# Kernel tuning notes

Measured on AMD Instinct MI355X. Metric: run time of the kernel, lower is better.

## Reference

```python
import jax, jax.numpy as jnp
import numpy as np

N_POINTS = 4096
N_PROJS = 2000


def setup_inputs() -> dict:
    key = jax.random.key(0)
    k1, k2, k3 = jax.random.split(key, 3)
    Xs = jax.random.normal(k1, (N_POINTS, 3), dtype=jnp.float32)
    Xt = jax.random.normal(k2, (N_POINTS, 3), dtype=jnp.float32)
    Us = jax.random.normal(k3, (N_PROJS, 3, 2), dtype=jnp.float32)
    return {"Xs": Xs, "Xt": Xt, "Us": Us}


def _project_to_circle(X, Us):
    # X: [n, d], Us: [P, d, 2] -> angles in [0, 1): [P, n]
    Xp = jnp.einsum('pdk,nd->pnk', Us, X)  # [P, n, 2]
    nrm = jnp.sqrt(jnp.sum(Xp * Xp, axis=-1, keepdims=True))
    Xp = Xp / jnp.maximum(nrm, 1e-12)  # F.normalize
    return (jnp.arctan2(-Xp[..., 1], -Xp[..., 0]) + np.pi) / (2 * np.pi)


def _emd1d_circle_p1(u_values, v_values):
    # Circular W1 via level-median (Delon et al.). u,v: [P, n], [P, m]
    P, n = u_values.shape
    m = v_values.shape[-1]
    dt = u_values.dtype
    u_w = jnp.full((P, n), 1.0 / n, dtype=dt)
    v_w = jnp.full((P, m), 1.0 / m, dtype=dt)
    us = jnp.sort(u_values, axis=-1)
    vs = jnp.sort(v_values, axis=-1)
    vals = jnp.concatenate([us, vs], axis=-1)            # [P, n+m]
    sorter = jnp.argsort(vals, axis=-1)
    vals_sorted = jnp.take_along_axis(vals, sorter, axis=-1)
    w_cat = jnp.concatenate([u_w, -v_w], axis=-1)
    cdf_diff = jnp.cumsum(jnp.take_along_axis(w_cat, sorter, axis=-1), axis=-1)
    cdf_sorter = jnp.argsort(cdf_diff, axis=-1)
    cdf_diff_sorted = jnp.take_along_axis(cdf_diff, cdf_sorter, axis=-1)
    vals_pad = jnp.concatenate([vals_sorted, jnp.ones((P, 1), dtype=dt)], axis=-1)
    delta = vals_pad[..., 1:] - vals_pad[..., :-1]
    weight_sorted = jnp.take_along_axis(delta, cdf_sorter, axis=-1)
    sum_weights = jnp.cumsum(weight_sorted, axis=-1) - 0.5
    sum_weights = jnp.where(sum_weights < 0, jnp.inf, sum_weights)
    inds = jnp.argmin(sum_weights, axis=-1)
    levMed = jnp.take_along_axis(cdf_diff_sorted, inds[:, None], axis=-1)  # [P, 1]
    return jnp.sum(delta * jnp.abs(cdf_diff - levMed), axis=-1)  # [P]


def reference(Xs, Xt, Us):
    Xps = _project_to_circle(Xs, Us)  # [P, n]
    Xpt = _project_to_circle(Xt, Us)  # [P, m]
    w1 = _emd1d_circle_p1(Xps, Xpt)
    return jnp.mean(w1)
```

## Files before the change

kernel.cpp:

```cpp
#include <hip/hip_runtime.h>
#include <math.h>

#define NPTS   4096
#define NPROJ  2000
#define NB     1024
#define NMERGE 8192
#define VPT    8

__device__ __forceinline__ int sw(int i) {
    return i ^ ((i >> 5) & 31);
}

__device__ __forceinline__ void local_merge(float v[VPT], bool asc) {
    #pragma unroll
    for (int j = 4; j >= 1; j >>= 1) {
        #pragma unroll
        for (int e = 0; e < VPT; ++e) {
            if ((e & j) == 0) {
                float a = v[e], b = v[e | j];
                float mn = fminf(a, b), mx = fmaxf(a, b);
                v[e]     = asc ? mn : mx;
                v[e | j] = asc ? mx : mn;
            }
        }
    }
}

__global__ __launch_bounds__(NB) void swd_kernel(
    const float* __restrict__ Xs, const float* __restrict__ Xt,
    const float* __restrict__ Us, float* __restrict__ out)
{
    __shared__ float keys[NMERGE];

    const int tid  = threadIdx.x;
    const int arr  = tid >> 9;
    const int c    = tid & 511;
    const int lane = tid & 63;
    const int wid  = tid >> 6;
    const int p    = blockIdx.x;

    const float u00 = Us[p*6+0], u01 = Us[p*6+1];
    const float u10 = Us[p*6+2], u11 = Us[p*6+3];
    const float u20 = Us[p*6+4], u21 = Us[p*6+5];

    const float pi_f   = 3.14159265358979323846f;
    const float inv2pi = 0.15915494309189535f;

    const float* __restrict__ X = arr ? Xt : Xs;

    float v[VPT];
    {
        const float4* X4 = (const float4*)(X + c * (VPT * 3));
        #pragma unroll
        for (int t = 0; t < 2; ++t) {
            float4 q0 = X4[t*3+0], q1 = X4[t*3+1], q2 = X4[t*3+2];
            #define ANG(x,y,z) ((atan2f(-((x)*u01+(y)*u11+(z)*u21), \
                                        -((x)*u00+(y)*u10+(z)*u20)) + pi_f) * inv2pi)
            v[t*4+0] = ANG(q0.x, q0.y, q0.z);
            v[t*4+1] = ANG(q0.w, q1.x, q1.y);
            v[t*4+2] = ANG(q1.z, q1.w, q2.x);
            v[t*4+3] = ANG(q2.y, q2.z, q2.w);
            #undef ANG
        }
    }

    #pragma unroll
    for (int k = 2; k <= 4; k <<= 1) {
        #pragma unroll
        for (int j = k >> 1; j >= 1; j >>= 1) {
            #pragma unroll
            for (int e = 0; e < VPT; ++e) {
                if ((e & j) == 0) {
                    bool asc = ((e & k) == 0);
                    float a = v[e], b = v[e | j];
                    float mn = fminf(a, b), mx = fmaxf(a, b);
                    v[e]     = asc ? mn : mx;
                    v[e | j] = asc ? mx : mn;
                }
            }
        }
    }

    local_merge(v, (c & 1) == 0);

    #pragma unroll
    for (int k = 16; k <= 512; k <<= 1) {
        bool asc = (k == 512) || ((c & (k >> 3)) == 0);
        #pragma unroll
        for (int d = k >> 4; d >= 1; d >>= 1) {
            bool keepmin = (((c & d) == 0) == asc);
            #pragma unroll
            for (int e = 0; e < VPT; ++e) {
                float o = __shfl_xor(v[e], d, 64);
                v[e] = keepmin ? fminf(v[e], o) : fmaxf(v[e], o);
            }
        }
        local_merge(v, asc);
    }

    #pragma unroll
    for (int e = 0; e < VPT; ++e) keys[sw(tid * VPT + e)] = v[e];
    __syncthreads();

    #define MERGE_ROUND(L, AB, DD)                                          \
    {                                                                       \
        const int Ab = (AB);                                                \
        const int Bb = Ab + (L);                                            \
        const int dd = (DD);                                                \
        int lo = dd > (L) ? dd - (L) : 0;                                   \
        int hi = dd < (L) ? dd : (L);                                       \
        while (lo < hi) {                                                   \
            int mid = (lo + hi) >> 1;                                       \
            if (keys[sw(Ab + mid)] <= keys[sw(Bb + (dd - 1 - mid))])        \
                lo = mid + 1; else hi = mid;                                \
        }                                                                   \
        int i = lo, j = dd - lo;                                            \
        const float INFV = __builtin_inff();                                \
        float cu = (i < (L)) ? keys[sw(Ab + i)] : INFV;                     \
        float cv = (j < (L)) ? keys[sw(Bb + j)] : INFV;                     \
        _Pragma("unroll")                                                   \
        for (int s = 0; s < VPT; ++s) {                                     \
            bool take = (cu <= cv);                                         \
            v[s] = fminf(cu, cv);                                           \
            if (take) { ++i; cu = (i < (L)) ? keys[sw(Ab + i)] : INFV; }    \
            else      { ++j; cv = (j < (L)) ? keys[sw(Bb + j)] : INFV; }    \
        }                                                                   \
        __syncthreads();                                                    \
        _Pragma("unroll")                                                   \
        for (int e = 0; e < VPT; ++e) keys[sw(tid * VPT + e)] = v[e];       \
        __syncthreads();                                                    \
    }

    MERGE_ROUND(512,  arr * 4096 + (c >> 7) * 1024, (c & 127) * VPT)
    MERGE_ROUND(1024, arr * 4096 + (c >> 8) * 2048, (c & 255) * VPT)
    MERGE_ROUND(2048, arr * 4096,                   c * VPT)
    #undef MERGE_ROUND

    int c_init;
    int offmin = 16, offmax = -16;
    float offf[VPT];
    {
        const int d0 = tid * VPT;
        int lo = d0 > NPTS ? d0 - NPTS : 0;
        int hi = d0 < NPTS ? d0 : NPTS;
        while (lo < hi) {
            int mid = (lo + hi) >> 1;
            if (keys[sw(mid)] <= keys[sw(NPTS + (d0 - 1 - mid))]) lo = mid + 1; else hi = mid;
        }
        int i = lo, j = d0 - lo;
        c_init = i - j;
        const float FMAXV = 3.402823466e+38f;
        float cu = (i < NPTS) ? keys[sw(i)] : FMAXV;
        float cv = (j < NPTS) ? keys[sw(NPTS + j)] : FMAXV;
        #pragma unroll
        for (int s = 0; s < VPT; ++s) {
            float cur;
            if (cu <= cv) { cur = cu; ++i; cu = (i < NPTS) ? keys[sw(i)] : FMAXV; }
            else          { cur = cv; ++j; cv = (j < NPTS) ? keys[sw(NPTS + j)] : FMAXV; }
            float nxt = fminf(cu, cv);
            if (nxt == FMAXV) nxt = 1.0f;
            v[s] = nxt - cur;
            int off = (i - j) - c_init;
            offmin = min(offmin, off);
            offmax = max(offmax, off);
            offf[s] = (float)off;
        }
    }

    __syncthreads();
    int*   ired = (int*)keys;
    float* red  = keys + 32;
    float* wred = keys + 48;

    int cmn = c_init + offmin, cmx = c_init + offmax;
    #pragma unroll
    for (int o = 32; o >= 1; o >>= 1) {
        cmn = min(cmn, __shfl_xor(cmn, o, 64));
        cmx = max(cmx, __shfl_xor(cmx, o, 64));
    }
    if (lane == 0) { ired[wid] = cmn; ired[16 + wid] = cmx; }
    if (tid < 16) red[tid] = 0.0f;
    __syncthreads();
    cmn = ired[0]; cmx = ired[16];
    #pragma unroll
    for (int w = 1; w < 16; ++w) {
        cmn = min(cmn, ired[w]);
        cmx = max(cmx, ired[16 + w]);
    }

    int lo_c = cmn - 1, hi_c = cmx;
    int it = 0;
    #pragma unroll 1
    while (hi_c - lo_c > 1) {
        const int mid = (lo_c + hi_c) >> 1;
        const float thrf = (float)(mid - c_init);
        float s_loc = 0.0f;
        #pragma unroll
        for (int s = 0; s < VPT; ++s)
            s_loc += (offf[s] <= thrf) ? v[s] : 0.0f;
        #pragma unroll
        for (int o = 32; o >= 1; o >>= 1) s_loc += __shfl_down(s_loc, o, 64);
        if (lane == 0) atomicAdd(&red[it], s_loc);
        __syncthreads();
        float S = red[it];
        if (S >= 0.5f) hi_c = mid; else lo_c = mid;
        ++it;
    }
    const int cstar = hi_c;

    float part = 0.0f;
    {
        const float thrf = (float)(cstar - c_init);
        #pragma unroll
        for (int s = 0; s < VPT; ++s)
            part += v[s] * fabsf(offf[s] - thrf);
    }
    #pragma unroll
    for (int o = 32; o >= 1; o >>= 1) part += __shfl_down(part, o, 64);
    if (lane == 0) wred[wid] = part;
    __syncthreads();
    if (tid == 0) {
        float w1 = 0.0f;
        #pragma unroll
        for (int w = 0; w < 16; ++w) w1 += wred[w];
        w1 *= (1.0f / 4096.0f);
        atomicAdd(out, w1 * (1.0f / (float)NPROJ));
    }
}

extern "C" void kernel_launch(void* const* d_in, const int* in_sizes, int n_in,
                              void* d_out, int out_size, void* d_ws, size_t ws_size,
                              hipStream_t stream) {
    const float* Xs = (const float*)d_in[0];
    const float* Xt = (const float*)d_in[1];
    const float* Us = (const float*)d_in[2];
    float* out = (float*)d_out;

    hipMemsetAsync(out, 0, sizeof(float), stream);
    swd_kernel<<<NPROJ, NB, 0, stream>>>(Xs, Xt, Us, out);
}
```

Before: 222.2 us.

## Double-buffer shared merge arrays and make merge-path loads branchless

Replaces the single shared key buffer with two ping-pong buffers, so each merge round reads from one and writes to the other. This removes one barrier per round and the barrier before the reduction scratch reuse. The merge-path step loops now do a single unconditional masked LDS load with selects instead of divergent branches with two load sites. The cost is doubling LDS to 64KB per block, which may limit residency on the CU.

Measured after the change: 217.8 us. 2.0% less time.

```diff
diff --git a/kernel.cpp b/kernel.cpp
--- a/kernel.cpp
+++ b/kernel.cpp
@@ -30,7 +30,8 @@
     const float* __restrict__ Xs, const float* __restrict__ Xt,
     const float* __restrict__ Us, float* __restrict__ out)
 {
-    __shared__ float keys[NMERGE];
+    __shared__ float bufA[NMERGE];
+    __shared__ float bufB[NMERGE];
 
     const int tid  = threadIdx.x;
     const int arr  = tid >> 9;
@@ -99,10 +100,10 @@
     }
 
     #pragma unroll
-    for (int e = 0; e < VPT; ++e) keys[sw(tid * VPT + e)] = v[e];
+    for (int e = 0; e < VPT; ++e) bufA[sw(tid * VPT + e)] = v[e];
     __syncthreads();
 
-    #define MERGE_ROUND(L, AB, DD)                                          \
+    #define MERGE_ROUND(SRC, DST, L, AB, DD)                                \
     {                                                                       \
         const int Ab = (AB);                                                \
         const int Bb = Ab + (L);                                            \
@@ -111,29 +112,33 @@
         int hi = dd < (L) ? dd : (L);                                       \
         while (lo < hi) {                                                   \
             int mid = (lo + hi) >> 1;                                       \
-            if (keys[sw(Ab + mid)] <= keys[sw(Bb + (dd - 1 - mid))])        \
+            if (SRC[sw(Ab + mid)] <= SRC[sw(Bb + (dd - 1 - mid))])          \
                 lo = mid + 1; else hi = mid;                                \
         }                                                                   \
         int i = lo, j = dd - lo;                                            \
         const float INFV = __builtin_inff();                                \
-        float cu = (i < (L)) ? keys[sw(Ab + i)] : INFV;                     \
-        float cv = (j < (L)) ? keys[sw(Bb + j)] : INFV;                     \
+        float cu = (i < (L)) ? SRC[sw(Ab + i)] : INFV;                      \
+        float cv = (j < (L)) ? SRC[sw(Bb + j)] : INFV;                      \
         _Pragma("unroll")                                                   \
         for (int s = 0; s < VPT; ++s) {                                     \
             bool take = (cu <= cv);                                         \
             v[s] = fminf(cu, cv);                                           \
-            if (take) { ++i; cu = (i < (L)) ? keys[sw(Ab + i)] : INFV; }    \
-            else      { ++j; cv = (j < (L)) ? keys[sw(Bb + j)] : INFV; }    \
+            i += take; j += !take;                                          \
+            int sel  = take ? i : j;                                        \
+            int badd = (take ? (Ab + i) : (Bb + j)) & (NMERGE - 1);         \
+            float tmp = SRC[sw(badd)];                                      \
+            float val = (sel < (L)) ? tmp : INFV;                           \
+            cu = take ? val : cu;                                           \
+            cv = take ? cv : val;                                           \
         }                                                                   \
+        _Pragma("unroll")                                                   \
+        for (int e = 0; e < VPT; ++e) DST[sw(tid * VPT + e)] = v[e];        \
         __syncthreads();                                                    \
-        _Pragma("unroll")                                                   \
-        for (int e = 0; e < VPT; ++e) keys[sw(tid * VPT + e)] = v[e];       \
-        __syncthreads();                                                    \
-    }
-
-    MERGE_ROUND(512,  arr * 4096 + (c >> 7) * 1024, (c & 127) * VPT)
-    MERGE_ROUND(1024, arr * 4096 + (c >> 8) * 2048, (c & 255) * VPT)
-    MERGE_ROUND(2048, arr * 4096,                   c * VPT)
+    }
+
+    MERGE_ROUND(bufA, bufB, 512,  arr * 4096 + (c >> 7) * 1024, (c & 127) * VPT)
+    MERGE_ROUND(bufB, bufA, 1024, arr * 4096 + (c >> 8) * 2048, (c & 255) * VPT)
+    MERGE_ROUND(bufA, bufB, 2048, arr * 4096,                   c * VPT)
     #undef MERGE_ROUND
 
     int c_init;
@@ -145,18 +150,24 @@
         int hi = d0 < NPTS ? d0 : NPTS;
         while (lo < hi) {
             int mid = (lo + hi) >> 1;
-            if (keys[sw(mid)] <= keys[sw(NPTS + (d0 - 1 - mid))]) lo = mid + 1; else hi = mid;
+            if (bufB[sw(mid)] <= bufB[sw(NPTS + (d0 - 1 - mid))]) lo = mid + 1; else hi = mid;
         }
         int i = lo, j = d0 - lo;
         c_init = i - j;
         const float FMAXV = 3.402823466e+38f;
-        float cu = (i < NPTS) ? keys[sw(i)] : FMAXV;
-        float cv = (j < NPTS) ? keys[sw(NPTS + j)] : FMAXV;
+        float cu = (i < NPTS) ? bufB[sw(i)] : FMAXV;
+        float cv = (j < NPTS) ? bufB[sw(NPTS + j)] : FMAXV;
         #pragma unroll
         for (int s = 0; s < VPT; ++s) {
-            float cur;
-            if (cu <= cv) { cur = cu; ++i; cu = (i < NPTS) ? keys[sw(i)] : FMAXV; }
-            else          { cur = cv; ++j; cv = (j < NPTS) ? keys[sw(NPTS + j)] : FMAXV; }
+            bool take = (cu <= cv);
+            float cur = fminf(cu, cv);
+            i += take; j += !take;
+            int sel  = take ? i : j;
+            int badd = (take ? i : (NPTS + j)) & (NMERGE - 1);
+            float tmp = bufB[sw(badd)];
+            float val = (sel < NPTS) ? tmp : FMAXV;
+            cu = take ? val : cu;
+            cv = take ? cv : val;
             float nxt = fminf(cu, cv);
             if (nxt == FMAXV) nxt = 1.0f;
             v[s] = nxt - cur;
@@ -167,10 +178,9 @@
         }
     }
 
-    __syncthreads();
-    int*   ired = (int*)keys;
-    float* red  = keys + 32;
-    float* wred = keys + 48;
+    int*   ired = (int*)bufA;
+    float* red  = bufA + 32;
+    float* wred = bufA + 48;
 
     int cmn = c_init + offmin, cmx = c_init + offmax;
     #pragma unroll
```
